# Kernel optimization log

Hardware: AMD Instinct MI355X
Metric: run time of the kernel (lower is better)

## Reference

```python
import jax, jax.numpy as jnp
import numpy as np

B, E, H, W = 32, 512, 16, 16
NH, HD = 8, 64          # num_heads = embed_dim // num_heads_channels, head_dim = 64
OUT = 512
S = H * W + 1           # spacial_dim**2 + 1 = 257 (mean token prepended)


def setup_inputs() -> dict:
    key = jax.random.key(0)
    ks = jax.random.split(key, 10)
    sc = 1.0 / np.sqrt(E).astype(np.float32)
    n = lambda k, sh, s=1.0: jax.random.normal(k, sh, jnp.float32) * s
    return {
        "x_real": n(ks[0], (B, E, H, W)),
        "x_imag": n(ks[1], (B, E, H, W)),
        # positional_embedding = (randn/sqrt(E)).to(complex64) -> imag part is zero
        "pos_r": n(ks[2], (E, S), sc),
        "pos_i": jnp.zeros((E, S), jnp.float32),
        # complex in-projection (packed q,k,v) and out-projection of the MHA
        "w_in_r": n(ks[3], (3 * E, E), sc),
        "w_in_i": n(ks[4], (3 * E, E), sc),
        "b_in_r": jnp.zeros((3 * E,), jnp.float32),
        "b_in_i": jnp.zeros((3 * E,), jnp.float32),
        "w_out_r": n(ks[5], (E, E), sc),
        "w_out_i": n(ks[6], (E, E), sc),
        "b_out_r": jnp.zeros((E,), jnp.float32),
        "b_out_i": jnp.zeros((E,), jnp.float32),
        # complex 1x1 conv projection == complex linear over channels
        "w_p_r": n(ks[7], (OUT, E), sc),
        "w_p_i": n(ks[8], (OUT, E), sc),
        "b_p_r": jnp.zeros((OUT,), jnp.float32),
        "b_p_i": jnp.zeros((OUT,), jnp.float32),
    }


def _attention_pool(x_real, x_imag, pos_r, pos_i, w_in_r, w_in_i, b_in_r, b_in_i,
                    w_out_r, w_out_i, b_out_r, b_out_i, w_p_r, w_p_i, b_p_r, b_p_i):
    cx = jax.lax.complex
    x = cx(x_real, x_imag).reshape(B, E, -1)                       # [b,c,HW]
    x = jnp.concatenate([x.mean(-1, keepdims=True), x], axis=-1)   # [b,c,S]
    x = x + cx(pos_r, pos_i)[None]                                 # + pos embed
    x = x.transpose(0, 2, 1)                                       # [b,S,E]

    qkv = jnp.einsum('bse,fe->bsf', x, cx(w_in_r, w_in_i)) + cx(b_in_r, b_in_i)
    q, k, v = jnp.split(qkv, 3, axis=-1)
    q = q.reshape(B, S, NH, HD) / jnp.sqrt(jnp.float32(HD))
    k = k.reshape(B, S, NH, HD)
    v = v.reshape(B, S, NH, HD)

    logits = jnp.einsum('bqhd,bkhd->bhqk', q, k)                   # complex scores
    # complex softmax handled separately on real/imag parts
    w = cx(jax.nn.softmax(logits.real, axis=-1),
           jax.nn.softmax(logits.imag, axis=-1))
    attn = jnp.einsum('bhqk,bkhd->bqhd', w, v).reshape(B, S, E)
    attn = jnp.einsum('bse,fe->bsf', attn, cx(w_out_r, w_out_i)) + cx(b_out_r, b_out_i)

    y = attn.transpose(0, 2, 1)                                    # [b,E,S]
    y = jnp.einsum('oc,bcs->bos', cx(w_p_r, w_p_i), y) + cx(b_p_r, b_p_i)[None, :, None]
    return y[:, :, 0]                                              # [b,OUT] complex64


def reference(x_real, x_imag, pos_r, pos_i, w_in_r, w_in_i, b_in_r, b_in_i,
              w_out_r, w_out_i, b_out_r, b_out_i, w_p_r, w_p_i, b_p_r, b_p_i):
    return _attention_pool(x_real, x_imag, pos_r, pos_i, w_in_r, w_in_i, b_in_r,
                           b_in_i, w_out_r, w_out_i, b_out_r, b_out_i,
                           w_p_r, w_p_i, b_p_r, b_p_i)
```

## Files before the change

kernel.cpp:

```cpp
#include <hip/hip_runtime.h>

#define B_   32
#define E_   512
#define HW_  256
#define S_   257
#define NH_  8
#define HD_  64
#define EC_  32
#define NCH_ (E_ / EC_)
#define NBLK 1024
#define NTHR 256
#define NWAVE (NBLK * (NTHR / 64))
#define NGRP 32
#define GSZ  32
#define BAR_STRIDE 2080

__device__ __forceinline__ void st_sys(float* p, float v) {
  __hip_atomic_store(p, v, __ATOMIC_RELAXED, __HIP_MEMORY_SCOPE_SYSTEM);
}
__device__ __forceinline__ void st_sys2(float2* p, float2 v) {
  unsigned long long u;
  __builtin_memcpy(&u, &v, 8);
  __hip_atomic_store((unsigned long long*)p, u, __ATOMIC_RELAXED, __HIP_MEMORY_SCOPE_SYSTEM);
}

__device__ __forceinline__ float wave_reduce(float v) {
  #pragma unroll
  for (int o = 32; o > 0; o >>= 1) v += __shfl_down(v, o, 64);
  return v;
}

__device__ __forceinline__ void gsync(unsigned* base, int bid, int t) {
  __syncthreads();
  if (t == 0) {
    int g = bid >> 5;
    unsigned* gcnt  = base + g * 32;
    unsigned* gctr  = base + NGRP * 32;
    unsigned* gflag = base + (NGRP + 1) * 32 + g * 32;
    if (__hip_atomic_fetch_add(gcnt, 1u, __ATOMIC_RELAXED, __HIP_MEMORY_SCOPE_AGENT) == GSZ - 1) {
      if (__hip_atomic_fetch_add(gctr, 1u, __ATOMIC_RELAXED, __HIP_MEMORY_SCOPE_AGENT) == NGRP - 1) {
        #pragma unroll
        for (int i = 0; i < NGRP; ++i)
          __hip_atomic_store(base + (NGRP + 1) * 32 + i * 32, 1u,
                             __ATOMIC_RELAXED, __HIP_MEMORY_SCOPE_SYSTEM);
      }
    }
    while (__hip_atomic_load(gflag, __ATOMIC_RELAXED, __HIP_MEMORY_SCOPE_SYSTEM) == 0u)
      __builtin_amdgcn_s_sleep(8);
  }
  __syncthreads();
}

__device__ void softmax257(float* l, float* red, int t) {
  float v = l[t];
  float v256 = l[256];
  red[t] = v; __syncthreads();
  #pragma unroll
  for (int s = 128; s > 0; s >>= 1) { if (t < s) red[t] = fmaxf(red[t], red[t + s]); __syncthreads(); }
  float M = fmaxf(red[0], v256);
  __syncthreads();
  float ex = expf(v - M);
  float e256 = expf(v256 - M);
  red[t] = ex; __syncthreads();
  #pragma unroll
  for (int s = 128; s > 0; s >>= 1) { if (t < s) red[t] += red[t + s]; __syncthreads(); }
  float inv = 1.f / (red[0] + e256);
  __syncthreads();
  l[t] = ex * inv;
  if (t == 0) l[256] = e256 * inv;
  __syncthreads();
}

__global__ __launch_bounds__(NTHR, 4) void k_mega(
    const float* __restrict__ xr, const float* __restrict__ xi,
    const float* __restrict__ pos_r, const float* __restrict__ pos_i,
    const float* __restrict__ w_in_r, const float* __restrict__ w_in_i,
    const float* __restrict__ b_in_r, const float* __restrict__ b_in_i,
    const float* __restrict__ w_out_r, const float* __restrict__ w_out_i,
    const float* __restrict__ b_out_r, const float* __restrict__ b_out_i,
    const float* __restrict__ w_p_r, const float* __restrict__ w_p_i,
    const float* __restrict__ b_p_r, const float* __restrict__ b_p_i,
    unsigned* bar,
    float* __restrict__ mr, float* __restrict__ mi,
    float* __restrict__ ur, float* __restrict__ ui,
    float* __restrict__ l0r, float* __restrict__ l0i,
    float* __restrict__ part, float* __restrict__ w2,
    float* __restrict__ zr_, float* __restrict__ zi_,
    float* __restrict__ a0r, float* __restrict__ a0i,
    float* __restrict__ aor, float* __restrict__ aoi,
    float* __restrict__ out, int interleaved) {
  __shared__ __align__(16) float smF[4112];
  const int t   = threadIdx.x;
  const int l   = t & 63;
  const int w   = t >> 6;
  const int bid = blockIdx.x;
  const int gw  = bid * 4 + w;

  #pragma unroll
  for (int j = 0; j < 4; ++j) {
    int task = gw + j * NWAVE;
    int e = task & (E_ - 1);
    float4 vr = ((const float4*)(xr + (size_t)task * HW_))[l];
    float4 vi = ((const float4*)(xi + (size_t)task * HW_))[l];
    float sr = (vr.x + vr.y) + (vr.z + vr.w);
    float si = (vi.x + vi.y) + (vi.z + vi.w);
    sr = wave_reduce(sr); si = wave_reduce(si);
    if (l == 0) {
      st_sys(&mr[task], sr * (1.f / HW_) + pos_r[(size_t)e * S_]);
      st_sys(&mi[task], si * (1.f / HW_) + pos_i[(size_t)e * S_]);
    }
  }
  gsync(bar + 0 * BAR_STRIDE, bid, t);

  if (bid < B_ * NH_) {
    int b = bid >> 3, h = bid & 7;
    float* mR  = smF;
    float* mI  = smF + 512;
    float* q0R = smF + 1024;
    float* q0I = smF + 1088;
    float* red = smF + 1152;
    mR[t]       = mr[b * E_ + t];        mI[t]       = mi[b * E_ + t];
    mR[t + 256] = mr[b * E_ + t + 256];  mI[t + 256] = mi[b * E_ + t + 256];
    __syncthreads();
    for (int j2 = 0; j2 < 16; ++j2) {
      int d = w * 16 + j2;
      int f = h * HD_ + d;
      const float* wr = w_in_r + (size_t)f * E_;
      const float* wi = w_in_i + (size_t)f * E_;
      float ar = 0.f, ai = 0.f;
      #pragma unroll
      for (int e = l; e < E_; e += 64) {
        float Xr = mR[e], Xi = mI[e], Cr = wr[e], Ci = wi[e];
        ar += Xr * Cr - Xi * Ci;
        ai += Xr * Ci + Xi * Cr;
      }
      ar = wave_reduce(ar); ai = wave_reduce(ai);
      if (l == 0) {
        q0R[d] = (ar + b_in_r[f]) * 0.125f;
        q0I[d] = (ai + b_in_i[f]) * 0.125f;
      }
    }
    __syncthreads();
    float u0r = 0.f, u0i = 0.f, u1r = 0.f, u1i = 0.f;
    #pragma unroll 8
    for (int d = 0; d < HD_; ++d) {
      float qr = q0R[d], qi = q0I[d];
      const float* Wr = w_in_r + (size_t)(E_ + h * HD_ + d) * E_;
      const float* Wi = w_in_i + (size_t)(E_ + h * HD_ + d) * E_;
      float W0r = Wr[t], W0i = Wi[t], W1r = Wr[t + 256], W1i = Wi[t + 256];
      u0r += qr * W0r - qi * W0i;  u0i += qr * W0i + qi * W0r;
      u1r += qr * W1r - qi * W1i;  u1i += qr * W1i + qi * W1r;
    }
    st_sys(&ur[(size_t)bid * E_ + t], u0r);        st_sys(&ui[(size_t)bid * E_ + t], u0i);
    st_sys(&ur[(size_t)bid * E_ + t + 256], u1r);  st_sys(&ui[(size_t)bid * E_ + t + 256], u1i);
    float pr = mR[t] * u0r - mI[t] * u0i + mR[t + 256] * u1r - mI[t + 256] * u1i;
    float pi = mR[t] * u0i + mI[t] * u0r + mR[t + 256] * u1i + mI[t + 256] * u1r;
    red[t] = pr; __syncthreads();
    #pragma unroll
    for (int s = 128; s > 0; s >>= 1) { if (t < s) red[t] += red[t + s]; __syncthreads(); }
    if (t == 0) st_sys(&l0r[bid], red[0]);
    __syncthreads();
    red[t] = pi; __syncthreads();
    #pragma unroll
    for (int s = 128; s > 0; s >>= 1) { if (t < s) red[t] += red[t + s]; __syncthreads(); }
    if (t == 0) st_sys(&l0i[bid], red[0]);
  }
  gsync(bar + 1 * BAR_STRIDE, bid, t);

  if (bid < B_ * NCH_) {
    int b = bid / NCH_, c = bid % NCH_;
    int e0 = c * EC_;
    float* us = smF;
    { int e = t >> 3, hh = t & 7;
      us[(e * 8 + hh) * 2 + 0] = ur[(size_t)(b * NH_ + hh) * E_ + e0 + e];
      us[(e * 8 + hh) * 2 + 1] = ui[(size_t)(b * NH_ + hh) * E_ + e0 + e]; }
    __syncthreads();
    float ar[NH_], ai[NH_];
    #pragma unroll
    for (int hh = 0; hh < NH_; ++hh) { ar[hh] = 0.f; ai[hh] = 0.f; }
    const float* xrb = xr + ((size_t)b * E_ + e0) * HW_;
    const float* xib = xi + ((size_t)b * E_ + e0) * HW_;
    #pragma unroll 2
    for (int e = 0; e < EC_; ++e) {
      float Xr = xrb[e * HW_ + t] + pos_r[(size_t)(e0 + e) * S_ + t + 1];
      float Xi = xib[e * HW_ + t] + pos_i[(size_t)(e0 + e) * S_ + t + 1];
      #pragma unroll
      for (int hh = 0; hh < NH_; ++hh) {
        float Ur = us[(e * 8 + hh) * 2 + 0], Ui = us[(e * 8 + hh) * 2 + 1];
        ar[hh] += Xr * Ur - Xi * Ui;
        ai[hh] += Xr * Ui + Xi * Ur;
      }
    }
    float2* p2 = (float2*)part;
    #pragma unroll
    for (int hh = 0; hh < NH_; ++hh) {
      float2 v; v.x = ar[hh]; v.y = ai[hh];
      st_sys2(&p2[((size_t)(b * NH_ + hh) * NCH_ + c) * 256 + t], v);
    }
  }
  gsync(bar + 2 * BAR_STRIDE, bid, t);

  if (bid < B_ * NH_) {
    int bh = bid;
    float* lr  = smF;
    float* li  = smF + 260;
    float* red = smF + 520;
    const float2* p2 = (const float2*)part + (size_t)bh * NCH_ * 256;
    float sr = 0.f, si = 0.f;
    #pragma unroll
    for (int c = 0; c < NCH_; ++c) { float2 v = p2[c * 256 + t]; sr += v.x; si += v.y; }
    lr[t + 1] = sr; li[t + 1] = si;
    if (t == 0) { lr[0] = l0r[bh]; li[0] = l0i[bh]; }
    __syncthreads();
    softmax257(lr, red, t);
    softmax257(li, red, t);
    float2* o = (float2*)w2 + (size_t)bh * S_;
    float2 v; v.x = lr[t]; v.y = li[t];
    st_sys2(&o[t], v);
    if (t == 0) { float2 v2; v2.x = lr[256]; v2.y = li[256]; st_sys2(&o[256], v2); }
  }
  gsync(bar + 3 * BAR_STRIDE, bid, t);

  {
    int b = bid >> 5, gg = bid & 31;
    float2* wls = (float2*)smF;
    const float2* w2b = (const float2*)w2 + (size_t)b * NH_ * S_;
    for (int i = t; i < NH_ * S_; i += NTHR) wls[i] = w2b[i];
    __syncthreads();
    #pragma unroll
    for (int sub = 0; sub < 2; ++sub) {
      int g = gg + sub * 32;
      #pragma unroll
      for (int r = 0; r < 2; ++r) {
        int e = g * 8 + w * 2 + r;
        const float* xre = xr + ((size_t)b * E_ + e) * HW_;
        const float* xie = xi + ((size_t)b * E_ + e) * HW_;
        const float* pre = pos_r + (size_t)e * S_;
        const float* pie = pos_i + (size_t)e * S_;
        float ar2[NH_], ai2[NH_];
        #pragma unroll
        for (int hh = 0; hh < NH_; ++hh) { ar2[hh] = 0.f; ai2[hh] = 0.f; }
        #pragma unroll
        for (int j = 0; j < 4; ++j) {
          int k = 1 + l + 64 * j;
          float Xr = xre[k - 1] + pre[k];
          float Xi = xie[k - 1] + pie[k];
          #pragma unroll
          for (int hh = 0; hh < NH_; ++hh) {
            float2 W = wls[hh * S_ + k];
            ar2[hh] += W.x * Xr - W.y * Xi;
            ai2[hh] += W.x * Xi + W.y * Xr;
          }
        }
        #pragma unroll
        for (int hh = 0; hh < NH_; ++hh) { ar2[hh] = wave_reduce(ar2[hh]); ai2[hh] = wave_reduce(ai2[hh]); }
        if (l == 0) {
          float X0r = mr[b * E_ + e];
          float X0i = mi[b * E_ + e];
          #pragma unroll
          for (int hh = 0; hh < NH_; ++hh) {
            float2 W0 = wls[hh * S_];
            st_sys(&zr_[(size_t)(b * NH_ + hh) * E_ + e], ar2[hh] + W0.x * X0r - W0.y * X0i);
            st_sys(&zi_[(size_t)(b * NH_ + hh) * E_ + e], ai2[hh] + W0.x * X0i + W0.y * X0r);
          }
        }
      }
    }
  }
  gsync(bar + 4 * BAR_STRIDE, bid, t);

  #pragma unroll
  for (int j = 0; j < 4; ++j) {
    int wid = gw + j * NWAVE;
    int b = wid >> 9, f = wid & (E_ - 1);
    int h = f >> 6;
    const float* wrp = w_in_r + (size_t)(2 * E_ + f) * E_;
    const float* wip = w_in_i + (size_t)(2 * E_ + f) * E_;
    const float* zrp = zr_ + (size_t)(b * NH_ + h) * E_;
    const float* zip = zi_ + (size_t)(b * NH_ + h) * E_;
    float ar = 0.f, ai = 0.f;
    #pragma unroll
    for (int e = l; e < E_; e += 64) {
      float Zr = zrp[e], Zi = zip[e], Cr = wrp[e], Ci = wip[e];
      ar += Zr * Cr - Zi * Ci;
      ai += Zr * Ci + Zi * Cr;
    }
    ar = wave_reduce(ar); ai = wave_reduce(ai);
    if (l == 0) {
      float bvr = b_in_r[2 * E_ + f], bvi = b_in_i[2 * E_ + f];
      st_sys(&a0r[wid], ar + (bvr - bvi));
      st_sys(&a0i[wid], ai + (bvr + bvi));
    }
  }
  gsync(bar + 5 * BAR_STRIDE, bid, t);

  #pragma unroll
  for (int j = 0; j < 4; ++j) {
    int wid = gw + j * NWAVE;
    int b = wid >> 9, f = wid & (E_ - 1);
    const float* wrp = w_out_r + (size_t)f * E_;
    const float* wip = w_out_i + (size_t)f * E_;
    const float* ir = a0r + (size_t)b * E_;
    const float* ii = a0i + (size_t)b * E_;
    float ar = 0.f, ai = 0.f;
    #pragma unroll
    for (int e = l; e < E_; e += 64) {
      float Xr = ir[e], Xi = ii[e], Cr = wrp[e], Ci = wip[e];
      ar += Xr * Cr - Xi * Ci;
      ai += Xr * Ci + Xi * Cr;
    }
    ar = wave_reduce(ar); ai = wave_reduce(ai);
    if (l == 0) { st_sys(&aor[wid], ar + b_out_r[f]); st_sys(&aoi[wid], ai + b_out_i[f]); }
  }
  gsync(bar + 6 * BAR_STRIDE, bid, t);

  #pragma unroll
  for (int j = 0; j < 4; ++j) {
    int wid = gw + j * NWAVE;
    int b = wid >> 9, f = wid & (E_ - 1);
    const float* wrp = w_p_r + (size_t)f * E_;
    const float* wip = w_p_i + (size_t)f * E_;
    const float* ir = aor + (size_t)b * E_;
    const float* ii = aoi + (size_t)b * E_;
    float ar = 0.f, ai = 0.f;
    #pragma unroll
    for (int e = l; e < E_; e += 64) {
      float Xr = ir[e], Xi = ii[e], Cr = wrp[e], Ci = wip[e];
      ar += Xr * Cr - Xi * Ci;
      ai += Xr * Ci + Xi * Cr;
    }
    ar = wave_reduce(ar); ai = wave_reduce(ai);
    if (l == 0) {
      float rr = ar + b_p_r[f];
      float im = ai + b_p_i[f];
      if (interleaved) { out[(size_t)wid * 2] = rr; out[(size_t)wid * 2 + 1] = im; }
      else             { out[wid] = rr; }
    }
  }
}

extern "C" void kernel_launch(void* const* d_in, const int* in_sizes, int n_in,
                              void* d_out, int out_size, void* d_ws, size_t ws_size,
                              hipStream_t stream) {
  (void)in_sizes; (void)n_in; (void)ws_size;
  const float* xr      = (const float*)d_in[0];
  const float* xi      = (const float*)d_in[1];
  const float* pos_r   = (const float*)d_in[2];
  const float* pos_i   = (const float*)d_in[3];
  const float* w_in_r  = (const float*)d_in[4];
  const float* w_in_i  = (const float*)d_in[5];
  const float* b_in_r  = (const float*)d_in[6];
  const float* b_in_i  = (const float*)d_in[7];
  const float* w_out_r = (const float*)d_in[8];
  const float* w_out_i = (const float*)d_in[9];
  const float* b_out_r = (const float*)d_in[10];
  const float* b_out_i = (const float*)d_in[11];
  const float* w_p_r   = (const float*)d_in[12];
  const float* w_p_i   = (const float*)d_in[13];
  const float* b_p_r   = (const float*)d_in[14];
  const float* b_p_i   = (const float*)d_in[15];

  const int BE = B_ * E_, BHE = B_ * NH_ * E_;
  unsigned* bar = (unsigned*)d_ws;
  float* base = (float*)d_ws + 16384;
  float* mr   = base;
  float* mi   = mr  + BE;
  float* ur   = mi  + BE;
  float* ui   = ur  + BHE;
  float* l0r  = ui  + BHE;
  float* l0i  = l0r + B_ * NH_;
  float* part = l0i + B_ * NH_;
  float* w2   = part + (size_t)B_ * NH_ * NCH_ * 512;
  float* zr   = w2  + (size_t)2 * B_ * NH_ * S_;
  float* zi   = zr  + BHE;
  float* a0r  = zi  + BHE;
  float* a0i  = a0r + BE;
  float* aor  = a0i + BE;
  float* aoi  = aor + BE;

  hipMemsetAsync(d_ws, 0, 65536, stream);
  k_mega<<<NBLK, NTHR, 0, stream>>>(
      xr, xi, pos_r, pos_i, w_in_r, w_in_i, b_in_r, b_in_i,
      w_out_r, w_out_i, b_out_r, b_out_i, w_p_r, w_p_i, b_p_r, b_p_i,
      bar, mr, mi, ur, ui, l0r, l0i, part, w2, zr, zi, a0r, a0i, aor, aoi,
      (float*)d_out, out_size >= 2 * B_ * E_);
}
```

Before: 196.9 us.

## Replace grid-wide barriers with per-batch group barriers and redistribute q/u work

Work is remapped so that each batch element is handled by its own group of 32 blocks, and every stage only depends on data from that batch. The global two-level atomic barrier is replaced by a per-group phase-slot barrier: each block writes its phase and one wave polls the group's 32 slots. The q0/u/l0 computation is also split across all 32 blocks of a group, with partial logits reduced later, instead of running in 256 blocks. This is meant to cut barrier latency and idle blocks, at the cost of extra partial-sum traffic and redundant loads of q0.

```diff
diff --git a/kernel.cpp b/kernel.cpp
--- a/kernel.cpp
+++ b/kernel.cpp
@@ -6,14 +6,12 @@
 #define S_   257
 #define NH_  8
 #define HD_  64
-#define EC_  32
-#define NCH_ (E_ / EC_)
+#define ECH_ 16
+#define NCH_ 32
 #define NBLK 1024
 #define NTHR 256
-#define NWAVE (NBLK * (NTHR / 64))
 #define NGRP 32
 #define GSZ  32
-#define BAR_STRIDE 2080
 
 __device__ __forceinline__ void st_sys(float* p, float v) {
   __hip_atomic_store(p, v, __ATOMIC_RELAXED, __HIP_MEMORY_SCOPE_SYSTEM);
@@ -30,23 +28,18 @@
   return v;
 }
 
-__device__ __forceinline__ void gsync(unsigned* base, int bid, int t) {
-  __syncthreads();
-  if (t == 0) {
-    int g = bid >> 5;
-    unsigned* gcnt  = base + g * 32;
-    unsigned* gctr  = base + NGRP * 32;
-    unsigned* gflag = base + (NGRP + 1) * 32 + g * 32;
-    if (__hip_atomic_fetch_add(gcnt, 1u, __ATOMIC_RELAXED, __HIP_MEMORY_SCOPE_AGENT) == GSZ - 1) {
-      if (__hip_atomic_fetch_add(gctr, 1u, __ATOMIC_RELAXED, __HIP_MEMORY_SCOPE_AGENT) == NGRP - 1) {
-        #pragma unroll
-        for (int i = 0; i < NGRP; ++i)
-          __hip_atomic_store(base + (NGRP + 1) * 32 + i * 32, 1u,
-                             __ATOMIC_RELAXED, __HIP_MEMORY_SCOPE_SYSTEM);
-      }
-    }
-    while (__hip_atomic_load(gflag, __ATOMIC_RELAXED, __HIP_MEMORY_SCOPE_SYSTEM) == 0u)
-      __builtin_amdgcn_s_sleep(8);
+__device__ __forceinline__ void gbar(unsigned* slots, int g, int j, int t, unsigned phase) {
+  __syncthreads();
+  if (t < 64) {
+    if (t == 0)
+      __hip_atomic_store(&slots[g * GSZ + j], phase, __ATOMIC_RELAXED, __HIP_MEMORY_SCOPE_SYSTEM);
+    const unsigned* line = slots + g * GSZ;
+    int sl = t & 31;
+    for (;;) {
+      unsigned v = __hip_atomic_load(&line[sl], __ATOMIC_RELAXED, __HIP_MEMORY_SCOPE_SYSTEM);
+      if (__all((int)(v >= phase))) break;
+      __builtin_amdgcn_s_sleep(2);
+    }
   }
   __syncthreads();
 }
@@ -80,10 +73,10 @@
     const float* __restrict__ b_out_r, const float* __restrict__ b_out_i,
     const float* __restrict__ w_p_r, const float* __restrict__ w_p_i,
     const float* __restrict__ b_p_r, const float* __restrict__ b_p_i,
-    unsigned* bar,
+    unsigned* slots,
     float* __restrict__ mr, float* __restrict__ mi,
-    float* __restrict__ ur, float* __restrict__ ui,
-    float* __restrict__ l0r, float* __restrict__ l0i,
+    float* __restrict__ q0r, float* __restrict__ q0i,
+    float* __restrict__ l0pr, float* __restrict__ l0pi,
     float* __restrict__ part, float* __restrict__ w2,
     float* __restrict__ zr_, float* __restrict__ zi_,
     float* __restrict__ a0r, float* __restrict__ a0i,
@@ -94,37 +87,33 @@
   const int l   = t & 63;
   const int w   = t >> 6;
   const int bid = blockIdx.x;
-  const int gw  = bid * 4 + w;
-
-  #pragma unroll
-  for (int j = 0; j < 4; ++j) {
-    int task = gw + j * NWAVE;
-    int e = task & (E_ - 1);
-    float4 vr = ((const float4*)(xr + (size_t)task * HW_))[l];
-    float4 vi = ((const float4*)(xi + (size_t)task * HW_))[l];
+  const int g   = bid >> 5;
+  const int j   = bid & 31;
+
+  #pragma unroll
+  for (int rr = 0; rr < 4; ++rr) {
+    int e = j * 16 + w * 4 + rr;
+    float4 vr = ((const float4*)(xr + ((size_t)g * E_ + e) * HW_))[l];
+    float4 vi = ((const float4*)(xi + ((size_t)g * E_ + e) * HW_))[l];
     float sr = (vr.x + vr.y) + (vr.z + vr.w);
     float si = (vi.x + vi.y) + (vi.z + vi.w);
     sr = wave_reduce(sr); si = wave_reduce(si);
     if (l == 0) {
-      st_sys(&mr[task], sr * (1.f / HW_) + pos_r[(size_t)e * S_]);
-      st_sys(&mi[task], si * (1.f / HW_) + pos_i[(size_t)e * S_]);
-    }
-  }
-  gsync(bar + 0 * BAR_STRIDE, bid, t);
-
-  if (bid < B_ * NH_) {
-    int b = bid >> 3, h = bid & 7;
-    float* mR  = smF;
-    float* mI  = smF + 512;
-    float* q0R = smF + 1024;
-    float* q0I = smF + 1088;
-    float* red = smF + 1152;
-    mR[t]       = mr[b * E_ + t];        mI[t]       = mi[b * E_ + t];
-    mR[t + 256] = mr[b * E_ + t + 256];  mI[t + 256] = mi[b * E_ + t + 256];
-    __syncthreads();
-    for (int j2 = 0; j2 < 16; ++j2) {
-      int d = w * 16 + j2;
-      int f = h * HD_ + d;
+      st_sys(&mr[g * E_ + e], sr * (1.f / HW_) + pos_r[(size_t)e * S_]);
+      st_sys(&mi[g * E_ + e], si * (1.f / HW_) + pos_i[(size_t)e * S_]);
+    }
+  }
+  gbar(slots, g, j, t, 1);
+
+  {
+    float* mR = smF;
+    float* mI = smF + 512;
+    mR[t]       = mr[g * E_ + t];        mI[t]       = mi[g * E_ + t];
+    mR[t + 256] = mr[g * E_ + t + 256];  mI[t + 256] = mi[g * E_ + t + 256];
+    __syncthreads();
+    #pragma unroll
+    for (int rr = 0; rr < 4; ++rr) {
+      int f = j * 16 + w * 4 + rr;
       const float* wr = w_in_r + (size_t)f * E_;
       const float* wi = w_in_i + (size_t)f * E_;
       float ar = 0.f, ai = 0.f;
@@ -136,57 +125,66 @@
       }
       ar = wave_reduce(ar); ai = wave_reduce(ai);
       if (l == 0) {
-        q0R[d] = (ar + b_in_r[f]) * 0.125f;
-        q0I[d] = (ai + b_in_i[f]) * 0.125f;
-      }
-    }
-    __syncthreads();
-    float u0r = 0.f, u0i = 0.f, u1r = 0.f, u1i = 0.f;
-    #pragma unroll 8
-    for (int d = 0; d < HD_; ++d) {
-      float qr = q0R[d], qi = q0I[d];
-      const float* Wr = w_in_r + (size_t)(E_ + h * HD_ + d) * E_;
-      const float* Wi = w_in_i + (size_t)(E_ + h * HD_ + d) * E_;
-      float W0r = Wr[t], W0i = Wi[t], W1r = Wr[t + 256], W1i = Wi[t + 256];
-      u0r += qr * W0r - qi * W0i;  u0i += qr * W0i + qi * W0r;
-      u1r += qr * W1r - qi * W1i;  u1i += qr * W1i + qi * W1r;
-    }
-    st_sys(&ur[(size_t)bid * E_ + t], u0r);        st_sys(&ui[(size_t)bid * E_ + t], u0i);
-    st_sys(&ur[(size_t)bid * E_ + t + 256], u1r);  st_sys(&ui[(size_t)bid * E_ + t + 256], u1i);
-    float pr = mR[t] * u0r - mI[t] * u0i + mR[t + 256] * u1r - mI[t + 256] * u1i;
-    float pi = mR[t] * u0i + mI[t] * u0r + mR[t + 256] * u1i + mI[t + 256] * u1r;
-    red[t] = pr; __syncthreads();
-    #pragma unroll
-    for (int s = 128; s > 0; s >>= 1) { if (t < s) red[t] += red[t + s]; __syncthreads(); }
-    if (t == 0) st_sys(&l0r[bid], red[0]);
-    __syncthreads();
-    red[t] = pi; __syncthreads();
-    #pragma unroll
-    for (int s = 128; s > 0; s >>= 1) { if (t < s) red[t] += red[t + s]; __syncthreads(); }
-    if (t == 0) st_sys(&l0i[bid], red[0]);
-  }
-  gsync(bar + 1 * BAR_STRIDE, bid, t);
-
-  if (bid < B_ * NCH_) {
-    int b = bid / NCH_, c = bid % NCH_;
-    int e0 = c * EC_;
-    float* us = smF;
-    { int e = t >> 3, hh = t & 7;
-      us[(e * 8 + hh) * 2 + 0] = ur[(size_t)(b * NH_ + hh) * E_ + e0 + e];
-      us[(e * 8 + hh) * 2 + 1] = ui[(size_t)(b * NH_ + hh) * E_ + e0 + e]; }
-    __syncthreads();
+        st_sys(&q0r[g * E_ + f], (ar + b_in_r[f]) * 0.125f);
+        st_sys(&q0i[g * E_ + f], (ai + b_in_i[f]) * 0.125f);
+      }
+    }
+  }
+  gbar(slots, g, j, t, 2);
+
+  {
+    int c = j, e0 = c * ECH_;
+    float* q0s = smF;
+    float* us  = smF + 1024;
+    float* mS  = smF + 1280;
+    { int f0 = t * 2;
+      q0s[f0 * 2 + 0]       = q0r[g * E_ + f0];
+      q0s[f0 * 2 + 1]       = q0i[g * E_ + f0];
+      q0s[(f0 + 1) * 2 + 0] = q0r[g * E_ + f0 + 1];
+      q0s[(f0 + 1) * 2 + 1] = q0i[g * E_ + f0 + 1];
+      if (t < ECH_) { mS[t * 2] = mr[g * E_ + e0 + t]; mS[t * 2 + 1] = mi[g * E_ + e0 + t]; }
+    }
+    __syncthreads();
+    if (t < 128) {
+      int e = t & 15, hh = t >> 4;
+      float ar = 0.f, ai = 0.f;
+      #pragma unroll 8
+      for (int d = 0; d < HD_; ++d) {
+        int f = hh * HD_ + d;
+        float qr = q0s[f * 2], qi = q0s[f * 2 + 1];
+        float Wr = w_in_r[(size_t)(E_ + f) * E_ + e0 + e];
+        float Wi = w_in_i[(size_t)(E_ + f) * E_ + e0 + e];
+        ar += qr * Wr - qi * Wi;
+        ai += qr * Wi + qi * Wr;
+      }
+      us[(e * 8 + hh) * 2 + 0] = ar;
+      us[(e * 8 + hh) * 2 + 1] = ai;
+    }
+    __syncthreads();
+    if (t < NH_) {
+      float pr = 0.f, pi = 0.f;
+      #pragma unroll
+      for (int e = 0; e < ECH_; ++e) {
+        float Xr = mS[e * 2], Xi = mS[e * 2 + 1];
+        float Ur = us[(e * 8 + t) * 2], Ui = us[(e * 8 + t) * 2 + 1];
+        pr += Xr * Ur - Xi * Ui;
+        pi += Xr * Ui + Xi * Ur;
+      }
+      st_sys(&l0pr[((size_t)g * NH_ + t) * NCH_ + c], pr);
+      st_sys(&l0pi[((size_t)g * NH_ + t) * NCH_ + c], pi);
+    }
     float ar[NH_], ai[NH_];
     #pragma unroll
     for (int hh = 0; hh < NH_; ++hh) { ar[hh] = 0.f; ai[hh] = 0.f; }
-    const float* xrb = xr + ((size_t)b * E_ + e0) * HW_;
-    const float* xib = xi + ((size_t)b * E_ + e0) * HW_;
+    const float* xrb = xr + ((size_t)g * E_ + e0) * HW_;
+    const float* xib = xi + ((size_t)g * E_ + e0) * HW_;
     #pragma unroll 2
-    for (int e = 0; e < EC_; ++e) {
+    for (int e = 0; e < ECH_; ++e) {
       float Xr = xrb[e * HW_ + t] + pos_r[(size_t)(e0 + e) * S_ + t + 1];
       float Xi = xib[e * HW_ + t] + pos_i[(size_t)(e0 + e) * S_ + t + 1];
       #pragma unroll
       for (int hh = 0; hh < NH_; ++hh) {
-        float Ur = us[(e * 8 + hh) * 2 + 0], Ui = us[(e * 8 + hh) * 2 + 1];
+        float Ur = us[(e * 8 + hh) * 2], Ui = us[(e * 8 + hh) * 2 + 1];
         ar[hh] += Xr * Ur - Xi * Ui;
         ai[hh] += Xr * Ui + Xi * Ur;
       }
@@ -195,13 +193,13 @@
     #pragma unroll
     for (int hh = 0; hh < NH_; ++hh) {
       float2 v; v.x = ar[hh]; v.y = ai[hh];
-      st_sys2(&p2[((size_t)(b * NH_ + hh) * NCH_ + c) * 256 + t], v);
-    }
-  }
-  gsync(bar + 2 * BAR_STRIDE, bid, t);
-
-  if (bid < B_ * NH_) {
-    int bh = bid;
+      st_sys2(&p2[(((size_t)g * NH_ + hh) * NCH_ + c) * 256 + t], v);
+    }
+  }
+  gbar(slots, g, j, t, 3);
+
+  if (j < NH_) {
+    int bh = g * NH_ + j;
     float* lr  = smF;
     float* li  = smF + 260;
     float* red = smF + 520;
@@ -210,7 +208,16 @@
     #pragma unroll
     for (int c = 0; c < NCH_; ++c) { float2 v = p2[c * 256 + t]; sr += v.x; si += v.y; }
     lr[t + 1] = sr; li[t + 1] = si;
-    if (t == 0) { lr[0] = l0r[bh]; li[0] = l0i[bh]; }
+    if (t < 64) {
+      float v = (t < NCH_) ? l0pr[(size_t)bh * NCH_ + t] : 0.f;
+      v = wave_reduce(v);
+      if (t == 0) lr[0] = v;
+    } else if (t < 128) {
+      int tt = t - 64;
+      float v = (tt < NCH_) ? l0pi[(size_t)bh * NCH_ + tt] : 0.f;
+      v = wave_reduce(v);
+      if (tt == 0) li[0] = v;
+    }
     __syncthreads();
     softmax257(lr, red, t);
     softmax257(li, red, t);
@@ -219,30 +226,29 @@
     st_sys2(&o[t], v);
     if (t == 0) { float2 v2; v2.x = lr[256]; v2.y = li[256]; st_sys2(&o[256], v2); }
   }
-  gsync(bar + 3 * BAR_STRIDE, bid, t);
+  gbar(slots, g, j, t, 4);
 
   {
-    int b = bid >> 5, gg = bid & 31;
     float2* wls = (float2*)smF;
-    const float2* w2b = (const float2*)w2 + (size_t)b * NH_ * S_;
+    const float2* w2b = (const float2*)w2 + (size_t)g * NH_ * S_;
     for (int i = t; i < NH_ * S_; i += NTHR) wls[i] = w2b[i];
     __syncthreads();
     #pragma unroll
     for (int sub = 0; sub < 2; ++sub) {
-      int g = gg + sub * 32;
+      int gq = j + sub * 32;
       #pragma unroll
       for (int r = 0; r < 2; ++r) {
-        int e = g * 8 + w * 2 + r;
-        const float* xre = xr + ((size_t)b * E_ + e) * HW_;
-        const float* xie = xi + ((size_t)b * E_ + e) * HW_;
+        int e = gq * 8 + w * 2 + r;
+        const float* xre = xr + ((size_t)g * E_ + e) * HW_;
+        const float* xie = xi + ((size_t)g * E_ + e) * HW_;
         const float* pre = pos_r + (size_t)e * S_;
         const float* pie = pos_i + (size_t)e * S_;
         float ar2[NH_], ai2[NH_];
         #pragma unroll
         for (int hh = 0; hh < NH_; ++hh) { ar2[hh] = 0.f; ai2[hh] = 0.f; }
         #pragma unroll
-        for (int j = 0; j < 4; ++j) {
-          int k = 1 + l + 64 * j;
+        for (int jj = 0; jj < 4; ++jj) {
+          int k = 1 + l + 64 * jj;
           float Xr = xre[k - 1] + pre[k];
           float Xi = xie[k - 1] + pie[k];
           #pragma unroll
@@ -255,29 +261,28 @@
         #pragma unroll
         for (int hh = 0; hh < NH_; ++hh) { ar2[hh] = wave_reduce(ar2[hh]); ai2[hh] = wave_reduce(ai2[hh]); }
         if (l == 0) {
-          float X0r = mr[b * E_ + e];
-          float X0i = mi[b * E_ + e];
+          float X0r = mr[g * E_ + e];
+          float X0i = mi[g * E_ + e];
           #pragma unroll
           for (int hh = 0; hh < NH_; ++hh) {
             float2 W0 = wls[hh * S_];
-            st_sys(&zr_[(size_t)(b * NH_ + hh) * E_ + e], ar2[hh] + W0.x * X0r - W0.y * X0i);
-            st_sys(&zi_[(size_t)(b * NH_ + hh) * E_ + e], ai2[hh] + W0.x * X0i + W0.y * X0r);
+            st_sys(&zr_[(size_t)(g * NH_ + hh) * E_ + e], ar2[hh] + W0.x * X0r - W0.y * X0i);
+            st_sys(&zi_[(size_t)(g * NH_ + hh) * E_ + e], ai2[hh] + W0.x * X0i + W0.y * X0r);
           }
         }
       }
     }
   }
-  gsync(bar + 4 * BAR_STRIDE, bid, t);
-
-  #pragma unroll
-  for (int j = 0; j < 4; ++j) {
-    int wid = gw + j * NWAVE;
-    int b = wid >> 9, f = wid & (E_ - 1);
+  gbar(slots, g, j, t, 5);
+
+  #pragma unroll
+  for (int rr = 0; rr < 4; ++rr) {
+    int f = j * 16 + w * 4 + rr;
     int h = f >> 6;
     const float* wrp = w_in_r + (size_t)(2 * E_ + f) * E_;
     const float* wip = w_in_i + (size_t)(2 * E_ + f) * E_;
-    const float* zrp = zr_ + (size_t)(b * NH_ + h) * E_;
-    const float* zip = zi_ + (size_t)(b * NH_ + h) * E_;
+    const float* zrp = zr_ + (size_t)(g * NH_ + h) * E_;
+    const float* zip = zi_ + (size_t)(g * NH_ + h) * E_;
     float ar = 0.f, ai = 0.f;
     #pragma unroll
     for (int e = l; e < E_; e += 64) {
@@ -288,20 +293,19 @@
     ar = wave_reduce(ar); ai = wave_reduce(ai);
     if (l == 0) {
       float bvr = b_in_r[2 * E_ + f], bvi = b_in_i[2 * E_ + f];
-      st_sys(&a0r[wid], ar + (bvr - bvi));
-      st_sys(&a0i[wid], ai + (bvr + bvi));
-    }
-  }
-  gsync(bar + 5 * BAR_STRIDE, bid, t);
-
-  #pragma unroll
-  for (int j = 0; j < 4; ++j) {
-    int wid = gw + j * NWAVE;
-    int b = wid >> 9, f = wid & (E_ - 1);
+      st_sys(&a0r[g * E_ + f], ar + (bvr - bvi));
+      st_sys(&a0i[g * E_ + f], ai + (bvr + bvi));
+    }
+  }
+  gbar(slots, g, j, t, 6);
+
+  #pragma unroll
+  for (int rr = 0; rr < 4; ++rr) {
+    int f = j * 16 + w * 4 + rr;
     const float* wrp = w_out_r + (size_t)f * E_;
     const float* wip = w_out_i + (size_t)f * E_;
-    const float* ir = a0r + (size_t)b * E_;
-    const float* ii = a0i + (size_t)b * E_;
+    const float* ir = a0r + (size_t)g * E_;
+    const float* ii = a0i + (size_t)g * E_;
     float ar = 0.f, ai = 0.f;
     #pragma unroll
     for (int e = l; e < E_; e += 64) {
@@ -310,18 +314,17 @@
       ai += Xr * Ci + Xi * Cr;
     }
     ar = wave_reduce(ar); ai = wave_reduce(ai);
-    if (l == 0) { st_sys(&aor[wid], ar + b_out_r[f]); st_sys(&aoi[wid], ai + b_out_i[f]); }
-  }
-  gsync(bar + 6 * BAR_STRIDE, bid, t);
-
-  #pragma unroll
-  for (int j = 0; j < 4; ++j) {
-    int wid = gw + j * NWAVE;
-    int b = wid >> 9, f = wid & (E_ - 1);
+    if (l == 0) { st_sys(&aor[g * E_ + f], ar + b_out_r[f]); st_sys(&aoi[g * E_ + f], ai + b_out_i[f]); }
+  }
+  gbar(slots, g, j, t, 7);
+
+  #pragma unroll
+  for (int rr = 0; rr < 4; ++rr) {
+    int f = j * 16 + w * 4 + rr;
     const float* wrp = w_p_r + (size_t)f * E_;
     const float* wip = w_p_i + (size_t)f * E_;
-    const float* ir = aor + (size_t)b * E_;
-    const float* ii = aoi + (size_t)b * E_;
+    const float* ir = aor + (size_t)g * E_;
+    const float* ii = aoi + (size_t)g * E_;
     float ar = 0.f, ai = 0.f;
     #pragma unroll
     for (int e = l; e < E_; e += 64) {
@@ -331,10 +334,11 @@
     }
     ar = wave_reduce(ar); ai = wave_reduce(ai);
     if (l == 0) {
-      float rr = ar + b_p_r[f];
-      float im = ai + b_p_i[f];
-      if (interleaved) { out[(size_t)wid * 2] = rr; out[(size_t)wid * 2 + 1] = im; }
-      else             { out[wid] = rr; }
+      float rr2 = ar + b_p_r[f];
+      float im  = ai + b_p_i[f];
+      int wid = g * E_ + f;
+      if (interleaved) { out[(size_t)wid * 2] = rr2; out[(size_t)wid * 2 + 1] = im; }
+      else             { out[wid] = rr2; }
     }
   }
 }
@@ -361,27 +365,27 @@
   const float* b_p_i   = (const float*)d_in[15];
 
   const int BE = B_ * E_, BHE = B_ * NH_ * E_;
-  unsigned* bar = (unsigned*)d_ws;
-  float* base = (float*)d_ws + 16384;
+  unsigned* slots = (unsigned*)d_ws;
+  float* base = (float*)d_ws + 1024;
   float* mr   = base;
-  float* mi   = mr  + BE;
-  float* ur   = mi  + BE;
-  float* ui   = ur  + BHE;
-  float* l0r  = ui  + BHE;
-  float* l0i  = l0r + B_ * NH_;
-  float* part = l0i + B_ * NH_;
+  float* mi   = mr   + BE;
+  float* q0r  = mi   + BE;
+  float* q0i  = q0r  + BE;
+  float* l0pr = q0i  + BE;
+  float* l0pi = l0pr + B_ * NH_ * NCH_;
+  float* part = l0pi + B_ * NH_ * NCH_;
   float* w2   = part + (size_t)B_ * NH_ * NCH_ * 512;
-  float* zr   = w2  + (size_t)2 * B_ * NH_ * S_;
-  float* zi   = zr  + BHE;
-  float* a0r  = zi  + BHE;
-  float* a0i  = a0r + BE;
-  float* aor  = a0i + BE;
-  float* aoi  = aor + BE;
-
-  hipMemsetAsync(d_ws, 0, 65536, stream);
+  float* zr   = w2   + (size_t)2 * B_ * NH_ * S_;
+  float* zi   = zr   + BHE;
+  float* a0r  = zi   + BHE;
+  float* a0i  = a0r  + BE;
+  float* aor  = a0i  + BE;
+  float* aoi  = aor  + BE;
+
+  hipMemsetAsync(d_ws, 0, 4096, stream);
   k_mega<<<NBLK, NTHR, 0, stream>>>(
       xr, xi, pos_r, pos_i, w_in_r, w_in_i, b_in_r, b_in_i,
       w_out_r, w_out_i, b_out_r, b_out_i, w_p_r, w_p_i, b_p_r, b_p_i,
-      bar, mr, mi, ur, ui, l0r, l0i, part, w2, zr, zi, a0r, a0i, aor, aoi,
+      slots, mr, mi, q0r, q0i, l0pr, l0pi, part, w2, zr, zi, a0r, a0i, aor, aoi,
       (float*)d_out, out_size >= 2 * B_ * E_);
 }
```

Result: slower. 202.3 us (+2.8%).
